# Performance work log

Measured on AMD Instinct MI355X. Metric: run time of the kernel, lower is better.

The kernel has to match this reference:

```python
import jax, jax.numpy as jnp
import numpy as np

D_MODEL = 1024
N_HEAD = 16
L, B = 2048, 2


def setup_inputs() -> dict:
    key = jax.random.key(0)
    ks = jax.random.split(key, 11)
    inp = {
        "q": jax.random.normal(ks[0], (L, B, D_MODEL), dtype=jnp.float32),
        "k": jax.random.normal(ks[1], (L, B, D_MODEL), dtype=jnp.float32),
        "v": jax.random.normal(ks[2], (L, B, D_MODEL), dtype=jnp.float32),
        "sph": jax.random.uniform(ks[3], (B, N_HEAD, L, L), dtype=jnp.float32),
        "mask": jax.random.randint(ks[4], (B, L, L), 0, 2, dtype=jnp.int32),
        # learned params (torch Linear stores W of shape [out, in]; y = x @ W.T)
        "Wq": jax.random.normal(ks[5], (D_MODEL, D_MODEL), dtype=jnp.float32) * (1.0 / np.sqrt(D_MODEL)),
        "Wk": jax.random.normal(ks[6], (D_MODEL, D_MODEL), dtype=jnp.float32) * (1.0 / np.sqrt(D_MODEL)),
        "Wv": jax.random.normal(ks[7], (D_MODEL, D_MODEL), dtype=jnp.float32) * (1.0 / np.sqrt(D_MODEL)),
        "Wfc": jax.random.normal(ks[8], (D_MODEL, D_MODEL), dtype=jnp.float32) * (1.0 / np.sqrt(D_MODEL)),
        "gamma": jnp.ones((D_MODEL,), dtype=jnp.float32),
        "beta": jnp.zeros((D_MODEL,), dtype=jnp.float32),
    }
    return inp


def reference(q, k, v, sph, mask, Wq, Wk, Wv, Wfc, gamma, beta):
    # q, k, v: [L, B, D]  ->  batch-first [B, L, D]
    n_head = N_HEAD
    Lq, Bb, D = q.shape
    d_k = D // n_head
    x_q = jnp.transpose(q, (1, 0, 2))
    x_k = jnp.transpose(k, (1, 0, 2))
    x_v = jnp.transpose(v, (1, 0, 2))
    residual = x_q  # [B, L, D]

    # projections (no bias), split heads: [B, H, L, d_k]
    qh = (x_q @ Wq.T).reshape(Bb, Lq, n_head, d_k).transpose(0, 2, 1, 3)
    kh = (x_k @ Wk.T).reshape(Bb, Lq, n_head, d_k).transpose(0, 2, 1, 3)
    vh = (x_v @ Wv.T).reshape(Bb, Lq, n_head, d_k).transpose(0, 2, 1, 3)

    scale = jnp.asarray(d_k, qh.dtype) ** 0.5
    attn = jnp.einsum('bhqd,bhkd->bhqk', qh / scale, kh)
    attn = attn * sph                                   # spatial decay modulation
    attn = jnp.where(mask[:, None, :, :] == 0, jnp.asarray(-1e9, attn.dtype), attn)
    p_attn = jax.nn.softmax(attn, axis=-1)              # dropout is identity in eval

    out = jnp.einsum('bhqk,bhkd->bhqd', p_attn, vh)     # [B, H, L, d_k]
    out = out.transpose(0, 2, 1, 3).reshape(Bb, Lq, D)
    out = out @ Wfc.T + residual                        # fc (no bias) + residual

    # LayerNorm(eps=1e-6)
    mu = jnp.mean(out, axis=-1, keepdims=True)
    var = jnp.var(out, axis=-1, keepdims=True)
    out = (out - mu) * jax.lax.rsqrt(var + 1e-6) * gamma + beta

    return jnp.transpose(out, (1, 0, 2)), p_attn
```

## Files before the change

kernel.cpp:

```cpp
#include <hip/hip_runtime.h>
#include <hip/hip_bf16.h>

#define LL 2048
#define BB 2
#define DD 1024
#define HH 16
#define DKk 64

typedef __attribute__((ext_vector_type(8))) short s8v;
typedef __attribute__((ext_vector_type(8))) unsigned short u8v;
typedef __attribute__((ext_vector_type(4))) float f4v;

__device__ __forceinline__ ushort f2b(float f){
  union { __hip_bfloat16 h; ushort u; } c; c.h = __float2bfloat16(f); return c.u;
}
__device__ __forceinline__ float b2f(ushort u){
  union { __hip_bfloat16 h; ushort u; } c; c.u = u; return __bfloat162float(c.h);
}

__global__ __launch_bounds__(256) void pack_x_kernel(
    const float* __restrict__ q, const float* __restrict__ k, const float* __restrict__ v,
    ushort* __restrict__ xq, ushort* __restrict__ xk, ushort* __restrict__ xv){
  int t = blockIdx.x*256 + threadIdx.x;
  int m = t >> 7;
  int dc = (t & 127) << 3;
  int b = m >> 11, l = m & (LL-1);
  size_t src = ((size_t)(l*BB + b) << 10) + dc;
  size_t dst = ((size_t)m << 10) + dc;
  #pragma unroll
  for (int i=0;i<3;++i){
    const float* ss = (i==0)?q:(i==1)?k:v;
    ushort* dd = (i==0)?xq:(i==1)?xk:xv;
    float4 a = *(const float4*)(ss+src);
    float4 bb = *(const float4*)(ss+src+4);
    u8v o;
    o[0]=f2b(a.x); o[1]=f2b(a.y); o[2]=f2b(a.z); o[3]=f2b(a.w);
    o[4]=f2b(bb.x);o[5]=f2b(bb.y);o[6]=f2b(bb.z);o[7]=f2b(bb.w);
    *(u8v*)(dd+dst) = o;
  }
}

__global__ __launch_bounds__(256) void pack_w_kernel(
    const float* __restrict__ Wq, const float* __restrict__ Wk,
    const float* __restrict__ Wv, const float* __restrict__ Wfc,
    ushort* __restrict__ wb){
  int t = blockIdx.x*256 + threadIdx.x;
  int which = t >> 17;
  size_t idx = (size_t)(t & 131071) << 3;
  const float* s = (which==0)?Wq:(which==1)?Wk:(which==2)?Wv:Wfc;
  float4 a = *(const float4*)(s+idx);
  float4 b4 = *(const float4*)(s+idx+4);
  u8v o;
  o[0]=f2b(a.x);o[1]=f2b(a.y);o[2]=f2b(a.z);o[3]=f2b(a.w);
  o[4]=f2b(b4.x);o[5]=f2b(b4.y);o[6]=f2b(b4.z);o[7]=f2b(b4.w);
  *(u8v*)(wb + ((size_t)which<<20) + idx) = o;
}

__device__ __forceinline__ void gemm_body(
    const ushort* __restrict__ A, const ushort* __restrict__ W,
    ushort* __restrict__ outb, float* __restrict__ outf, const float* __restrict__ resid,
    int mode, float scale){
  __shared__ ushort As[4096];
  __shared__ ushort Bs[4096];
  int tid = threadIdx.x;
  int w = tid>>6, lane = tid&63, lane15 = lane&15, g = lane>>4;
  int m0 = blockIdx.y<<7, n0 = blockIdx.x<<7;
  int wr = w>>1, wc = w&1;
  f4v z4 = {0.f,0.f,0.f,0.f};
  f4v acc[4][4];
  #pragma unroll
  for (int i=0;i<4;++i)
    #pragma unroll
    for (int j=0;j<4;++j) acc[i][j] = z4;

  int f0 = tid, f1 = 256 + tid;
  int r0 = f0>>2, c0 = (f0&3)<<3;
  int r1 = f1>>2, c1 = (f1&3)<<3;
  for (int k0=0; k0<1024; k0+=32){
    *(s8v*)&As[(r0<<5)+c0] = *(const s8v*)&A[((size_t)(m0+r0)<<10) + k0 + c0];
    *(s8v*)&As[(r1<<5)+c1] = *(const s8v*)&A[((size_t)(m0+r1)<<10) + k0 + c1];
    *(s8v*)&Bs[(r0<<5)+c0] = *(const s8v*)&W[((size_t)(n0+r0)<<10) + k0 + c0];
    *(s8v*)&Bs[(r1<<5)+c1] = *(const s8v*)&W[((size_t)(n0+r1)<<10) + k0 + c1];
    __syncthreads();
    s8v af[4], bf_[4];
    #pragma unroll
    for (int mi=0;mi<4;++mi) af[mi] = *(s8v*)&As[((wr*64 + mi*16 + lane15)<<5) + (g<<3)];
    #pragma unroll
    for (int ni=0;ni<4;++ni) bf_[ni] = *(s8v*)&Bs[((wc*64 + ni*16 + lane15)<<5) + (g<<3)];
    #pragma unroll
    for (int mi=0;mi<4;++mi)
      #pragma unroll
      for (int ni=0;ni<4;++ni)
        acc[mi][ni] = __builtin_amdgcn_mfma_f32_16x16x32_bf16(af[mi], bf_[ni], acc[mi][ni], 0,0,0);
    __syncthreads();
  }
  #pragma unroll
  for (int mi=0;mi<4;++mi){
    #pragma unroll
    for (int ni=0;ni<4;++ni){
      int mbase = m0 + wr*64 + mi*16 + (g<<2);
      int ncol  = n0 + wc*64 + ni*16 + lane15;
      if (mode==0){
        int b=mbase>>11, h=ncol>>6, j=ncol&63;
        size_t o = (((size_t)(b*HH+h)*LL + (mbase&2047))<<6) + j;
        #pragma unroll
        for (int r=0;r<4;++r) outb[o + ((size_t)r<<6)] = f2b(acc[mi][ni][r]*scale);
      } else if (mode==2){
        int b=mbase>>11, h=ncol>>6, j=ncol&63;
        ushort4 pk = make_ushort4(f2b(acc[mi][ni][0]), f2b(acc[mi][ni][1]),
                                  f2b(acc[mi][ni][2]), f2b(acc[mi][ni][3]));
        *(ushort4*)&outb[(((size_t)(b*HH+h)*DKk + j)<<11) + (mbase&2047)] = pk;
      } else {
        int b=mbase>>11, l2=mbase&2047;
        #pragma unroll
        for (int r=0;r<4;++r)
          outf[((size_t)(mbase+r)<<10)+ncol] =
              acc[mi][ni][r] + resid[((size_t)((l2+r)*BB + b)<<10) + ncol];
      }
    }
  }
}

__global__ __launch_bounds__(256) void gemm_qkv_kernel(
    const ushort* __restrict__ xq, const ushort* __restrict__ xk, const ushort* __restrict__ xv,
    const ushort* __restrict__ wb, ushort* __restrict__ Qh, ushort* __restrict__ Kh, ushort* __restrict__ Vt){
  int z = blockIdx.z;
  const ushort* A = (z==0)?xq:(z==1)?xk:xv;
  const ushort* W = wb + ((size_t)z<<20);
  ushort* outb = (z==0)?Qh:(z==1)?Kh:Vt;
  int mode = (z==2)?2:0;
  float scale = (z==0)?0.125f:1.0f;
  gemm_body(A, W, outb, nullptr, nullptr, mode, scale);
}

__global__ __launch_bounds__(256) void gemm_fc_kernel(
    const ushort* __restrict__ ao, const ushort* __restrict__ wfc,
    const float* __restrict__ resid, float* __restrict__ fco){
  gemm_body(ao, wfc, nullptr, fco, resid, 3, 1.0f);
}

__global__ __launch_bounds__(1024) void attn_kernel(
    const ushort* __restrict__ Qh, const ushort* __restrict__ Kh, const ushort* __restrict__ Vt,
    const float* __restrict__ sph, const int* __restrict__ mask,
    float* __restrict__ p_out, ushort* __restrict__ attn_out){
  extern __shared__ char smem[];
  float* pbuf   = (float*)(smem + 65536);
  float* redsum = (float*)(smem + 65536 + 13056);
  int tid = threadIdx.x, w = tid>>6, lane = tid&63, lane15 = lane&15, g = lane>>4;
  int bid = blockIdx.x;
  int qt = bid & 127, h = (bid>>7)&15, b = bid>>11;
  int q0 = qt<<4;
  size_t bh = (size_t)b*HH + h;

  const ushort* Qbase = Qh + ((bh*LL + q0 + lane15)<<6) + (g<<3);
  s8v qa0 = *(const s8v*)Qbase;
  s8v qa1 = *(const s8v*)(Qbase + 32);
  #pragma unroll
  for (int cc=0; cc<8; ++cc){
    int c = (w<<3) + cc;
    const ushort* Kb = Kh + ((bh*LL + (c<<4) + lane15)<<6) + (g<<3);
    s8v kb0 = *(const s8v*)Kb;
    s8v kb1 = *(const s8v*)(Kb + 32);
    f4v cacc = {0.f,0.f,0.f,0.f};
    cacc = __builtin_amdgcn_mfma_f32_16x16x32_bf16(qa0, kb0, cacc, 0,0,0);
    cacc = __builtin_amdgcn_mfma_f32_16x16x32_bf16(qa1, kb1, cacc, 0,0,0);
    int colb = ((c<<4) + lane15) << 1;
    #pragma unroll
    for (int r=0;r<4;++r){
      int row = (g<<2)+r;
      *(ushort*)(smem + (row<<12) + (colb ^ ((row&7)<<4))) = f2b(cacc[r]);
    }
  }
  __syncthreads();

  int row = w;
  int qrow = q0 + row;
  const float* sph_r = sph + ((bh*LL + qrow)<<11);
  const int*  msk_r  = mask + (((size_t)b*LL + qrow)<<11);
  int rswz = (row&7)<<4;
  char* Srow = smem + (row<<12);
  float sum = 0.f;
  #pragma unroll
  for (int c2=0;c2<4;++c2){
    int col = (lane<<3) + (c2<<9);
    int boff = (col<<1) ^ rswz;
    s8v sv = *(s8v*)(Srow + boff);
    float4 p0 = *(const float4*)(sph_r + col);
    float4 p1 = *(const float4*)(sph_r + col + 4);
    int4 mk0 = *(const int4*)(msk_r + col);
    int4 mk1 = *(const int4*)(msk_r + col + 4);
    float e[8];
    e[0] = mk0.x ? __expf(b2f((ushort)sv[0])*p0.x) : 0.f;
    e[1] = mk0.y ? __expf(b2f((ushort)sv[1])*p0.y) : 0.f;
    e[2] = mk0.z ? __expf(b2f((ushort)sv[2])*p0.z) : 0.f;
    e[3] = mk0.w ? __expf(b2f((ushort)sv[3])*p0.w) : 0.f;
    e[4] = mk1.x ? __expf(b2f((ushort)sv[4])*p1.x) : 0.f;
    e[5] = mk1.y ? __expf(b2f((ushort)sv[5])*p1.y) : 0.f;
    e[6] = mk1.z ? __expf(b2f((ushort)sv[6])*p1.z) : 0.f;
    e[7] = mk1.w ? __expf(b2f((ushort)sv[7])*p1.w) : 0.f;
    u8v ov;
    #pragma unroll
    for (int j=0;j<8;++j){ ushort ue = f2b(e[j]); sum += b2f(ue); ov[j] = ue; }
    *(u8v*)(Srow + boff) = ov;
  }
  #pragma unroll
  for (int off=1; off<64; off<<=1) sum += __shfl_xor(sum, off, 64);
  if (lane==0) redsum[row] = sum;

  float inv = 1.0f / sum;
  float* prow_p = p_out + ((bh*LL + qrow)<<11);
  #pragma unroll
  for (int c2=0;c2<4;++c2){
    int col = (lane<<3) + (c2<<9);
    s8v sv = *(s8v*)(Srow + ((col<<1) ^ rswz));
    float4 o0, o1;
    o0.x=b2f((ushort)sv[0])*inv; o0.y=b2f((ushort)sv[1])*inv;
    o0.z=b2f((ushort)sv[2])*inv; o0.w=b2f((ushort)sv[3])*inv;
    o1.x=b2f((ushort)sv[4])*inv; o1.y=b2f((ushort)sv[5])*inv;
    o1.z=b2f((ushort)sv[6])*inv; o1.w=b2f((ushort)sv[7])*inv;
    *(float4*)(prow_p + col) = o0;
    *(float4*)(prow_p + col + 4) = o1;
  }
  __syncthreads();

  int ds = w & 3, kq = w >> 2;
  f4v oacc = {0.f,0.f,0.f,0.f};
  const ushort* Vb = Vt + ((bh*DKk + (ds<<4) + lane15)<<11) + (kq<<9) + (g<<3);
  char* Sa = smem + (lane15<<12);
  int aswz = (lane15&7)<<4;
  #pragma unroll
  for (int it=0; it<16; ++it){
    s8v pa = *(s8v*)(Sa + (((kq<<10) + (it<<6) + (g<<4)) ^ aswz));
    s8v vb = *(const s8v*)(Vb + (it<<5));
    oacc = __builtin_amdgcn_mfma_f32_16x16x32_bf16(pa, vb, oacc, 0,0,0);
  }
  if (kq){
    float* pp = pbuf + ((kq-1)*1088);
    #pragma unroll
    for (int r=0;r<4;++r) pp[((g<<2)+r)*68 + (ds<<4) + lane15] = oacc[r];
  }
  __syncthreads();
  if (kq==0){
    #pragma unroll
    for (int p=0;p<3;++p){
      float* pp = pbuf + p*1088;
      #pragma unroll
      for (int r=0;r<4;++r) oacc[r] += pp[((g<<2)+r)*68 + (ds<<4) + lane15];
    }
    #pragma unroll
    for (int r=0;r<4;++r){
      int qr = (g<<2)+r;
      float val = oacc[r] / redsum[qr];
      attn_out[((size_t)(b*LL + q0 + qr)<<10) + (h<<6) + (ds<<4) + lane15] = f2b(val);
    }
  }
}

__global__ __launch_bounds__(256) void ln_kernel(const float* __restrict__ fc,
    const float* __restrict__ gamma, const float* __restrict__ beta, float* __restrict__ out){
  __shared__ float rs[4], rq[4];
  int m = blockIdx.x, tid = threadIdx.x;
  int d0 = tid<<2;
  float4 x = *(const float4*)(fc + ((size_t)m<<10) + d0);
  float s = x.x+x.y+x.z+x.w;
  float sq = x.x*x.x+x.y*x.y+x.z*x.z+x.w*x.w;
  #pragma unroll
  for (int off=32; off; off>>=1){ s += __shfl_xor(s,off,64); sq += __shfl_xor(sq,off,64); }
  if ((tid&63)==0){ rs[tid>>6]=s; rq[tid>>6]=sq; }
  __syncthreads();
  float ts = rs[0]+rs[1]+rs[2]+rs[3];
  float tq = rq[0]+rq[1]+rq[2]+rq[3];
  float mu = ts*(1.0f/1024.0f);
  float var = tq*(1.0f/1024.0f) - mu*mu;
  float rr = rsqrtf(var + 1e-6f);
  float4 gm = *(const float4*)(gamma + d0);
  float4 bt = *(const float4*)(beta + d0);
  float4 y;
  y.x=(x.x-mu)*rr*gm.x+bt.x;
  y.y=(x.y-mu)*rr*gm.y+bt.y;
  y.z=(x.z-mu)*rr*gm.z+bt.z;
  y.w=(x.w-mu)*rr*gm.w+bt.w;
  int b=m>>11, l2=m&2047;
  *(float4*)(out + ((size_t)(l2*BB+b)<<10) + d0) = y;
}

extern "C" void kernel_launch(void* const* d_in, const int* in_sizes, int n_in,
                              void* d_out, int out_size, void* d_ws, size_t ws_size,
                              hipStream_t stream){
  const float* q    = (const float*)d_in[0];
  const float* k    = (const float*)d_in[1];
  const float* v    = (const float*)d_in[2];
  const float* sph  = (const float*)d_in[3];
  const int*   mask = (const int*)d_in[4];
  const float* Wq   = (const float*)d_in[5];
  const float* Wk   = (const float*)d_in[6];
  const float* Wv   = (const float*)d_in[7];
  const float* Wfc  = (const float*)d_in[8];
  const float* gamma= (const float*)d_in[9];
  const float* beta = (const float*)d_in[10];
  float* outp  = (float*)d_out;
  float* p_out = outp + 4194304;

  char* ws = (char*)d_ws;
  ushort* xq  = (ushort*)(ws);
  ushort* xk  = (ushort*)(ws + 8388608);
  ushort* xv  = (ushort*)(ws + 16777216);
  ushort* wb  = (ushort*)(ws + 25165824);
  ushort* Qh  = (ushort*)(ws + 33554432);
  ushort* Kh  = (ushort*)(ws + 41943040);
  ushort* Vt  = (ushort*)(ws + 50331648);
  ushort* ao  = (ushort*)(ws + 58720256);
  float*  fco = (float*)(ws + 67108864);

  pack_x_kernel<<<2048,256,0,stream>>>(q,k,v,xq,xk,xv);
  pack_w_kernel<<<2048,256,0,stream>>>(Wq,Wk,Wv,Wfc,wb);
  gemm_qkv_kernel<<<dim3(8,32,3),256,0,stream>>>(xq,xk,xv,wb,Qh,Kh,Vt);
  attn_kernel<<<4096,1024,78784,stream>>>(Qh,Kh,Vt,sph,mask,p_out,ao);
  gemm_fc_kernel<<<dim3(8,32),256,0,stream>>>(ao, wb + 3145728, q, fco);
  ln_kernel<<<4096,256,0,stream>>>(fco, gamma, beta, outp);
}
```

Measured before the change: 553.6 us.

## Bit-pack mask, prefetch K/V/sph, nontemporal sph/P traffic in attention

```diff
diff --git a/kernel.cpp b/kernel.cpp
--- a/kernel.cpp
+++ b/kernel.cpp
@@ -17,6 +17,8 @@
 __device__ __forceinline__ float b2f(ushort u){
   union { __hip_bfloat16 h; ushort u; } c; c.u = u; return __bfloat162float(c.h);
 }
+__device__ __forceinline__ f4v nt4(const float* p){ return __builtin_nontemporal_load((const f4v*)p); }
+__device__ __forceinline__ void nts4(float* p, f4v v){ __builtin_nontemporal_store(v, (f4v*)p); }
 
 __global__ __launch_bounds__(256) void pack_x_kernel(
     const float* __restrict__ q, const float* __restrict__ k, const float* __restrict__ v,
@@ -54,6 +56,16 @@
   o[0]=f2b(a.x);o[1]=f2b(a.y);o[2]=f2b(a.z);o[3]=f2b(a.w);
   o[4]=f2b(b4.x);o[5]=f2b(b4.y);o[6]=f2b(b4.z);o[7]=f2b(b4.w);
   *(u8v*)(wb + ((size_t)which<<20) + idx) = o;
+}
+
+__global__ __launch_bounds__(256) void pack_mask_kernel(
+    const int* __restrict__ mask, unsigned char* __restrict__ mbits){
+  int t = blockIdx.x*256 + threadIdx.x;
+  const int* src = mask + ((size_t)t<<3);
+  int4 a = *(const int4*)src; int4 b = *(const int4*)(src+4);
+  unsigned m = (a.x&1) | ((a.y&1)<<1) | ((a.z&1)<<2) | ((a.w&1)<<3)
+             | ((b.x&1)<<4) | ((b.y&1)<<5) | ((b.z&1)<<6) | ((b.w&1)<<7);
+  mbits[t] = (unsigned char)m;
 }
 
 __device__ __forceinline__ void gemm_body(
@@ -139,9 +151,9 @@
   gemm_body(ao, wfc, nullptr, fco, resid, 3, 1.0f);
 }
 
-__global__ __launch_bounds__(1024) void attn_kernel(
+__global__ __launch_bounds__(1024, 8) void attn_kernel(
     const ushort* __restrict__ Qh, const ushort* __restrict__ Kh, const ushort* __restrict__ Vt,
-    const float* __restrict__ sph, const int* __restrict__ mask,
+    const float* __restrict__ sph, const unsigned char* __restrict__ mbits,
     float* __restrict__ p_out, ushort* __restrict__ attn_out){
   extern __shared__ char smem[];
   float* pbuf   = (float*)(smem + 65536);
@@ -155,16 +167,20 @@
   const ushort* Qbase = Qh + ((bh*LL + q0 + lane15)<<6) + (g<<3);
   s8v qa0 = *(const s8v*)Qbase;
   s8v qa1 = *(const s8v*)(Qbase + 32);
+  const ushort* Kp = Kh + ((bh*LL + (w<<7) + lane15)<<6) + (g<<3);
+  s8v kb0n = *(const s8v*)Kp;
+  s8v kb1n = *(const s8v*)(Kp + 32);
   #pragma unroll
   for (int cc=0; cc<8; ++cc){
-    int c = (w<<3) + cc;
-    const ushort* Kb = Kh + ((bh*LL + (c<<4) + lane15)<<6) + (g<<3);
-    s8v kb0 = *(const s8v*)Kb;
-    s8v kb1 = *(const s8v*)(Kb + 32);
+    s8v kb0 = kb0n, kb1 = kb1n;
+    if (cc<7){
+      kb0n = *(const s8v*)(Kp + ((cc+1)<<10));
+      kb1n = *(const s8v*)(Kp + ((cc+1)<<10) + 32);
+    }
     f4v cacc = {0.f,0.f,0.f,0.f};
     cacc = __builtin_amdgcn_mfma_f32_16x16x32_bf16(qa0, kb0, cacc, 0,0,0);
     cacc = __builtin_amdgcn_mfma_f32_16x16x32_bf16(qa1, kb1, cacc, 0,0,0);
-    int colb = ((c<<4) + lane15) << 1;
+    int colb = (((w<<3)+cc)<<5) + (lane15<<1);
     #pragma unroll
     for (int r=0;r<4;++r){
       int row = (g<<2)+r;
@@ -176,32 +192,37 @@
   int row = w;
   int qrow = q0 + row;
   const float* sph_r = sph + ((bh*LL + qrow)<<11);
-  const int*  msk_r  = mask + (((size_t)b*LL + qrow)<<11);
+  const unsigned char* mb_r = mbits + (((size_t)b*LL + qrow)<<8);
   int rswz = (row&7)<<4;
   char* Srow = smem + (row<<12);
+  int colbase = lane<<3;
+  unsigned mw = (unsigned)mb_r[lane] | ((unsigned)mb_r[lane+64]<<8)
+              | ((unsigned)mb_r[lane+128]<<16) | ((unsigned)mb_r[lane+192]<<24);
+  f4v a0 = nt4(sph_r + colbase), a1 = nt4(sph_r + colbase + 4);
+  s8v svn = *(s8v*)(Srow + ((colbase<<1) ^ rswz));
   float sum = 0.f;
   #pragma unroll
   for (int c2=0;c2<4;++c2){
-    int col = (lane<<3) + (c2<<9);
-    int boff = (col<<1) ^ rswz;
-    s8v sv = *(s8v*)(Srow + boff);
-    float4 p0 = *(const float4*)(sph_r + col);
-    float4 p1 = *(const float4*)(sph_r + col + 4);
-    int4 mk0 = *(const int4*)(msk_r + col);
-    int4 mk1 = *(const int4*)(msk_r + col + 4);
+    f4v p0 = a0, p1 = a1; s8v sv = svn;
+    if (c2<3){
+      int ncol = colbase + ((c2+1)<<9);
+      a0 = nt4(sph_r + ncol); a1 = nt4(sph_r + ncol + 4);
+      svn = *(s8v*)(Srow + ((ncol<<1) ^ rswz));
+    }
+    unsigned m8 = (mw >> (c2*8));
     float e[8];
-    e[0] = mk0.x ? __expf(b2f((ushort)sv[0])*p0.x) : 0.f;
-    e[1] = mk0.y ? __expf(b2f((ushort)sv[1])*p0.y) : 0.f;
-    e[2] = mk0.z ? __expf(b2f((ushort)sv[2])*p0.z) : 0.f;
-    e[3] = mk0.w ? __expf(b2f((ushort)sv[3])*p0.w) : 0.f;
-    e[4] = mk1.x ? __expf(b2f((ushort)sv[4])*p1.x) : 0.f;
-    e[5] = mk1.y ? __expf(b2f((ushort)sv[5])*p1.y) : 0.f;
-    e[6] = mk1.z ? __expf(b2f((ushort)sv[6])*p1.z) : 0.f;
-    e[7] = mk1.w ? __expf(b2f((ushort)sv[7])*p1.w) : 0.f;
+    e[0] = (m8&1)   ? __expf(b2f((ushort)sv[0])*p0[0]) : 0.f;
+    e[1] = (m8&2)   ? __expf(b2f((ushort)sv[1])*p0[1]) : 0.f;
+    e[2] = (m8&4)   ? __expf(b2f((ushort)sv[2])*p0[2]) : 0.f;
+    e[3] = (m8&8)   ? __expf(b2f((ushort)sv[3])*p0[3]) : 0.f;
+    e[4] = (m8&16)  ? __expf(b2f((ushort)sv[4])*p1[0]) : 0.f;
+    e[5] = (m8&32)  ? __expf(b2f((ushort)sv[5])*p1[1]) : 0.f;
+    e[6] = (m8&64)  ? __expf(b2f((ushort)sv[6])*p1[2]) : 0.f;
+    e[7] = (m8&128) ? __expf(b2f((ushort)sv[7])*p1[3]) : 0.f;
     u8v ov;
     #pragma unroll
-    for (int j=0;j<8;++j){ ushort ue = f2b(e[j]); sum += b2f(ue); ov[j] = ue; }
-    *(u8v*)(Srow + boff) = ov;
+    for (int j=0;j<8;++j){ sum += e[j]; ov[j] = f2b(e[j]); }
+    *(u8v*)(Srow + (((colbase + (c2<<9))<<1) ^ rswz)) = ov;
   }
   #pragma unroll
   for (int off=1; off<64; off<<=1) sum += __shfl_xor(sum, off, 64);
@@ -209,17 +230,20 @@
 
   float inv = 1.0f / sum;
   float* prow_p = p_out + ((bh*LL + qrow)<<11);
+  s8v rv[4];
+  #pragma unroll
+  for (int c2=0;c2<4;++c2)
+    rv[c2] = *(s8v*)(Srow + (((colbase + (c2<<9))<<1) ^ rswz));
   #pragma unroll
   for (int c2=0;c2<4;++c2){
-    int col = (lane<<3) + (c2<<9);
-    s8v sv = *(s8v*)(Srow + ((col<<1) ^ rswz));
-    float4 o0, o1;
-    o0.x=b2f((ushort)sv[0])*inv; o0.y=b2f((ushort)sv[1])*inv;
-    o0.z=b2f((ushort)sv[2])*inv; o0.w=b2f((ushort)sv[3])*inv;
-    o1.x=b2f((ushort)sv[4])*inv; o1.y=b2f((ushort)sv[5])*inv;
-    o1.z=b2f((ushort)sv[6])*inv; o1.w=b2f((ushort)sv[7])*inv;
-    *(float4*)(prow_p + col) = o0;
-    *(float4*)(prow_p + col + 4) = o1;
+    int col = colbase + (c2<<9);
+    f4v o0, o1;
+    o0[0]=b2f((ushort)rv[c2][0])*inv; o0[1]=b2f((ushort)rv[c2][1])*inv;
+    o0[2]=b2f((ushort)rv[c2][2])*inv; o0[3]=b2f((ushort)rv[c2][3])*inv;
+    o1[0]=b2f((ushort)rv[c2][4])*inv; o1[1]=b2f((ushort)rv[c2][5])*inv;
+    o1[2]=b2f((ushort)rv[c2][6])*inv; o1[3]=b2f((ushort)rv[c2][7])*inv;
+    nts4(prow_p + col, o0);
+    nts4(prow_p + col + 4, o1);
   }
   __syncthreads();
 
@@ -228,10 +252,15 @@
   const ushort* Vb = Vt + ((bh*DKk + (ds<<4) + lane15)<<11) + (kq<<9) + (g<<3);
   char* Sa = smem + (lane15<<12);
   int aswz = (lane15&7)<<4;
+  s8v pan = *(s8v*)(Sa + (((kq<<10) + (g<<4)) ^ aswz));
+  s8v vbn = *(const s8v*)Vb;
   #pragma unroll
   for (int it=0; it<16; ++it){
-    s8v pa = *(s8v*)(Sa + (((kq<<10) + (it<<6) + (g<<4)) ^ aswz));
-    s8v vb = *(const s8v*)(Vb + (it<<5));
+    s8v pa = pan, vb = vbn;
+    if (it<15){
+      pan = *(s8v*)(Sa + (((kq<<10) + ((it+1)<<6) + (g<<4)) ^ aswz));
+      vbn = *(const s8v*)(Vb + ((it+1)<<5));
+    }
     oacc = __builtin_amdgcn_mfma_f32_16x16x32_bf16(pa, vb, oacc, 0,0,0);
   }
   if (kq){
@@ -311,11 +340,13 @@
   ushort* Vt  = (ushort*)(ws + 50331648);
   ushort* ao  = (ushort*)(ws + 58720256);
   float*  fco = (float*)(ws + 67108864);
+  unsigned char* mbits = (unsigned char*)(ws + 83886080);
 
   pack_x_kernel<<<2048,256,0,stream>>>(q,k,v,xq,xk,xv);
   pack_w_kernel<<<2048,256,0,stream>>>(Wq,Wk,Wv,Wfc,wb);
+  pack_mask_kernel<<<4096,256,0,stream>>>(mask, mbits);
   gemm_qkv_kernel<<<dim3(8,32,3),256,0,stream>>>(xq,xk,xv,wb,Qh,Kh,Vt);
-  attn_kernel<<<4096,1024,78784,stream>>>(Qh,Kh,Vt,sph,mask,p_out,ao);
+  attn_kernel<<<4096,1024,78784,stream>>>(Qh,Kh,Vt,sph,mbits,p_out,ao);
   gemm_fc_kernel<<<dim3(8,32),256,0,stream>>>(ao, wb + 3145728, q, fco);
   ln_kernel<<<4096,256,0,stream>>>(fco, gamma, beta, outp);
 }
```

Result: faster. 517.4 us (-6.5%).
